# Performance work log

Hardware: AMD Instinct MI355X
Metric: run time of the kernel (lower is better)

## Reference

```python
import jax, jax.numpy as jnp
import numpy as np

B, NA, NE = 1024, 15, 16
N_AGENTS = NA + 1
BN = B * N_AGENTS
D_OWN = D_ALL = D_EN = 32
H, NH, NMOVE, RD = 256, 4, 6, 8
HD = H // NH
GATE = 1.0
NEG = -1e9  # stand-in for -inf (safe under autodiff)


def _gelu(x):
    return jax.nn.gelu(x, approximate=False)  # torch nn.GELU default is exact


def _ln(x, g, b, eps=1e-5):
    m = x.mean(-1, keepdims=True)
    v = ((x - m) ** 2).mean(-1, keepdims=True)
    return (x - m) * jax.lax.rsqrt(v + eps) * g + b


def _masked_mean(x, mask, axis):
    w = mask[..., None].astype(x.dtype)
    return (x * w).sum(axis) / jnp.clip(w.sum(axis), 1e-8)


def _mha(q, kv, mask, Wq, Wk, Wv, Wo):
    # q: [BN,H], kv: [BN,M,H], mask: [BN,M] bool
    bn = q.shape[0]
    qh = (q @ Wq.T).reshape(bn, NH, HD)
    kh = (kv @ Wk.T).reshape(bn, -1, NH, HD)
    vh = (kv @ Wv.T).reshape(bn, -1, NH, HD)
    scores = jnp.einsum('bhd,bmhd->bhm', qh, kh) / np.sqrt(HD)
    scores = jnp.where(mask[:, None, :], scores, NEG)
    attn = jax.nn.softmax(scores, axis=-1)
    ctx = jnp.einsum('bhm,bmhd->bhd', attn, vh).reshape(bn, H)
    return ctx @ Wo.T


def setup_inputs() -> dict:
    key = jax.random.key(0)
    ks = iter(jax.random.split(key, 64))
    nrm = lambda *s: jax.random.normal(next(ks), s, dtype=jnp.float32)
    w = lambda o, i: nrm(o, i) * 0.02
    inp = dict(
        bs=B,
        own_feats=nrm(BN, 1, D_OWN),
        ally_feats=nrm(BN, NA, D_ALL),
        enemy_feats=nrm(BN, NE, D_EN),
        hidden_state=nrm(B, N_AGENTS, H),
        own_W=w(H, D_OWN), own_b=jnp.zeros(H),
        ally_W=w(H, D_ALL), ally_b=jnp.zeros(H),
        en_W=w(H, D_EN), en_b=jnp.zeros(H),
        aA_Wq=w(H, H), aA_Wk=w(H, H), aA_Wv=w(H, H), aA_Wo=w(H, H),
        aE_Wq=w(H, H), aE_Wk=w(H, H), aE_Wv=w(H, H), aE_Wo=w(H, H),
        fuse_W1=w(H, 3 * H), fuse_b1=jnp.zeros(H), fuse_g1=jnp.ones(H), fuse_be1=jnp.zeros(H),
        fuse_W2=w(H, H), fuse_b2=jnp.zeros(H),
        pool_W1=w(128, 3 * H), pool_b1=jnp.zeros(128), pool_g1=jnp.ones(128), pool_be1=jnp.zeros(128),
        pool_W2=w(128, 128), pool_b2=jnp.zeros(128),
        role_W1=w(128, 128), role_b1=jnp.zeros(128), role_g1=jnp.ones(128), role_be1=jnp.zeros(128),
        role_W2=w(RD, 128), role_b2=jnp.zeros(RD),
        rln_g=jnp.ones(RD), rln_b=jnp.zeros(RD),
        gru_Wih=w(3 * H, H + RD), gru_Whh=w(3 * H, H),
        gru_bih=jnp.zeros(3 * H), gru_bhh=jnp.zeros(3 * H),
        qn_W=w(NMOVE, H), qn_b=jnp.zeros(NMOVE),
        qp_W=w(H, H + RD), kp_W=w(H, H),
    )
    return inp


def reference(bs, own_feats, ally_feats, enemy_feats, hidden_state,
              own_W, own_b, ally_W, ally_b, en_W, en_b,
              aA_Wq, aA_Wk, aA_Wv, aA_Wo, aE_Wq, aE_Wk, aE_Wv, aE_Wo,
              fuse_W1, fuse_b1, fuse_g1, fuse_be1, fuse_W2, fuse_b2,
              pool_W1, pool_b1, pool_g1, pool_be1, pool_W2, pool_b2,
              role_W1, role_b1, role_g1, role_be1, role_W2, role_b2,
              rln_g, rln_b, gru_Wih, gru_Whh, gru_bih, gru_bhh,
              qn_W, qn_b, qp_W, kp_W):
    ally_mask = ~jnp.all(ally_feats == 0, axis=-1)   # [BN,Na]
    enemy_mask = ~jnp.all(enemy_feats == 0, axis=-1)  # [BN,Ne]

    own_e = own_feats @ own_W.T + own_b        # [BN,1,H]
    ally_e = ally_feats @ ally_W.T + ally_b    # [BN,Na,H]
    enemy_e = enemy_feats @ en_W.T + en_b      # [BN,Ne,H]
    self_emb = own_e[:, 0]                     # [BN,H]

    cA = _mha(self_emb, ally_e, ally_mask, aA_Wq, aA_Wk, aA_Wv, aA_Wo)
    cE = _mha(self_emb, enemy_e, enemy_mask, aE_Wq, aE_Wk, aE_Wv, aE_Wo)

    # fuse MLP: Linear -> GELU -> LN -> Linear
    f_in = jnp.concatenate([self_emb, cA, cE], axis=-1)
    h0 = _ln(_gelu(f_in @ fuse_W1.T + fuse_b1), fuse_g1, fuse_be1) @ fuse_W2.T + fuse_b2

    pA = _masked_mean(ally_e, ally_mask, 1)
    pE = _masked_mean(enemy_e, enemy_mask, 1)
    p_in = jnp.concatenate([self_emb, pA, pE], axis=-1)
    pooled = _ln(_gelu(p_in @ pool_W1.T + pool_b1), pool_g1, pool_be1) @ pool_W2.T + pool_b2
    r = jnp.tanh(_ln(_gelu(pooled @ role_W1.T + role_b1), role_g1, role_be1) @ role_W2.T + role_b2)
    r = _ln(r, rln_g, rln_b)

    # GRUCell (torch convention)
    h_prev = hidden_state.reshape(-1, H)
    x = jnp.concatenate([h0, GATE * r], axis=-1)
    gi = x @ gru_Wih.T + gru_bih
    gh = h_prev @ gru_Whh.T + gru_bhh
    i_r, i_z, i_n = jnp.split(gi, 3, axis=-1)
    h_r, h_z, h_n = jnp.split(gh, 3, axis=-1)
    rg = jax.nn.sigmoid(i_r + h_r)
    zg = jax.nn.sigmoid(i_z + h_z)
    ng = jnp.tanh(i_n + rg * h_n)
    h_cur = (1.0 - zg) * ng + zg * h_prev

    q_normal = h_cur @ qn_W.T + qn_b  # [BN,n_move]

    q_vec = jnp.concatenate([h_cur, GATE * r], axis=-1) @ qp_W.T  # [BN,H]
    k_vec = enemy_e @ kp_W.T                                       # [BN,Ne,H]
    logits = jnp.einsum('bj,bmj->bm', q_vec, k_vec) / np.sqrt(H)
    logits = jnp.where(enemy_mask, logits, NEG)
    denom = jnp.clip(enemy_mask.sum(-1, keepdims=True), 1).astype(logits.dtype)
    mean_valid = jnp.where(enemy_mask, logits, 0.0).sum(-1, keepdims=True) / denom
    q_interact = logits - mean_valid

    Q = jnp.concatenate([q_normal, q_interact], axis=-1)
    h_out = h_cur.reshape(bs, N_AGENTS, H)
    return Q, h_out
```

## Files before the change

kernel.cpp:

```cpp
#include <hip/hip_runtime.h>
#include <hip/hip_bf16.h>


#define MROWS 16384

typedef __attribute__((ext_vector_type(8))) short short8;
typedef __attribute__((ext_vector_type(4))) float float4v;
typedef __attribute__((ext_vector_type(4))) unsigned short ushort4v;
typedef __attribute__((ext_vector_type(2))) unsigned short ushort2v;

__device__ __forceinline__ unsigned short f2b(float f) {
    __hip_bfloat16 h = __float2bfloat16(f);
    return *reinterpret_cast<unsigned short*>(&h);
}
__device__ __forceinline__ float b2f(unsigned short u) {
    __hip_bfloat16 h;
    *reinterpret_cast<unsigned short*>(&h) = u;
    return __bfloat162float(h);
}
__device__ __forceinline__ void gll16(const unsigned short* g, unsigned short* l) {
    __builtin_amdgcn_global_load_lds((const __attribute__((address_space(1))) void*)g,
                                     (__attribute__((address_space(3))) void*)l, 16, 0, 0);
}

__global__ void cvt_misc(const float* __restrict__ hidden, const float* __restrict__ ownf,
                         unsigned short* __restrict__ XG, unsigned short* __restrict__ OWNb,
                         unsigned short* __restrict__ zbuf) {
    int idx = blockIdx.x * 256 + threadIdx.x;
    const int nh = MROWS * 64;
    const int no = MROWS * 8;
    if (idx < nh) {
        int row = idx >> 6, c4 = (idx & 63) * 4;
        float4 v = *(const float4*)(hidden + (size_t)row * 256 + c4);
        ushort4v d = { f2b(v.x), f2b(v.y), f2b(v.z), f2b(v.w) };
        *(ushort4v*)(XG + (size_t)row * 520 + 264 + c4) = d;
    } else if (idx < nh + no) {
        int j = idx - nh;
        int row = j >> 3, c4 = (j & 7) * 4;
        float4 v = *(const float4*)(ownf + (size_t)row * 32 + c4);
        ushort4v d = { f2b(v.x), f2b(v.y), f2b(v.z), f2b(v.w) };
        *(ushort4v*)(OWNb + (size_t)row * 32 + c4) = d;
    } else if (idx < nh + no + 16) {
        int j = idx - nh - no;
        ((uint4*)zbuf)[j] = make_uint4(0u, 0u, 0u, 0u);
    }
}

struct TOp {
    int type;
    const float* A; int sAi, sAk;
    const float* B; int sBj, sBk;
    void* O; int sOi;
    int I, J, K;
    int nb; int aB, bB, oB;
};
struct TOpSet { int n; int tiles[26]; TOp ops[26]; };

__global__ __launch_bounds__(256)
void compose_tiled(TOpSet S) {
    int t = blockIdx.x;
    int op = 0;
    while (op < S.n && t >= S.tiles[op]) { t -= S.tiles[op]; op++; }
    if (op >= S.n) return;
    TOp o = S.ops[op];
    int ti = (o.I + 31) >> 5, tj = (o.J + 31) >> 5;
    int per = ti * tj;
    int b = t / per;
    int rem = t - b * per;
    int i0 = (rem / tj) * 32, j0 = (rem % tj) * 32;
    int tid = threadIdx.x;
    if (o.type >= 2) {
        for (int e = tid; e < 1024; e += 256) {
            int r = e >> 5, c = e & 31;
            int i = i0 + r, j = j0 + c;
            if (i < o.I && j < o.J) {
                unsigned short v = 0;
                if (o.type == 2) v = f2b(o.A[(long)b * o.aB + (long)i * o.sAi + (long)j * o.sAk]);
                ((unsigned short*)o.O)[(long)b * o.oB + (long)i * o.sOi + j] = v;
            }
        }
        return;
    }
    __shared__ float As[32][33];
    __shared__ float Bs[32][33];
    int tx = tid & 15, ty = tid >> 4;
    float a00 = 0.f, a01 = 0.f, a10 = 0.f, a11 = 0.f;
    const float* Ab = o.A + (long)b * o.aB;
    const float* Bb = o.B + (long)b * o.bB;
    for (int k0 = 0; k0 < o.K; k0 += 32) {
        for (int e = tid; e < 1024; e += 256) {
            int r = e >> 5, c = e & 31;
            As[r][c] = (i0 + r < o.I && k0 + c < o.K)
                       ? Ab[(long)(i0 + r) * o.sAi + (long)(k0 + c) * o.sAk] : 0.f;
            Bs[r][c] = (k0 + r < o.K && j0 + c < o.J)
                       ? Bb[(long)(j0 + c) * o.sBj + (long)(k0 + r) * o.sBk] : 0.f;
        }
        __syncthreads();
#pragma unroll
        for (int k = 0; k < 32; k++) {
            float x0 = As[ty * 2][k], x1 = As[ty * 2 + 1][k];
            float y0 = Bs[k][tx * 2], y1 = Bs[k][tx * 2 + 1];
            a00 += x0 * y0; a01 += x0 * y1; a10 += x1 * y0; a11 += x1 * y1;
        }
        __syncthreads();
    }
    int i = i0 + ty * 2, j = j0 + tx * 2;
    float vals[2][2] = {{a00, a01}, {a10, a11}};
#pragma unroll
    for (int di = 0; di < 2; di++)
#pragma unroll
        for (int dj = 0; dj < 2; dj++) {
            int ii = i + di, jj = j + dj;
            if (ii < o.I && jj < o.J) {
                long oidx = (long)b * o.oB + (long)ii * o.sOi + jj;
                if (o.type == 0) ((unsigned short*)o.O)[oidx] = f2b(vals[di][dj]);
                else ((float*)o.O)[oidx] = vals[di][dj];
            }
        }
}

struct MOp { const float* A; int sAi; const float* x; const float* b1; const float* b2; float* out; int I, K; };
struct MOpSet { int n; int waves[10]; MOp ops[10]; };

__global__ void mv_ops(MOpSet S) {
    int wid = blockIdx.x * 4 + (threadIdx.x >> 6);
    int lane = threadIdx.x & 63;
    int op = 0;
    while (op < S.n && wid >= S.waves[op]) { wid -= S.waves[op]; op++; }
    if (op >= S.n) return;
    MOp o = S.ops[op];
    float s = 0.f;
    for (int k = lane; k < o.K; k += 64) s += o.A[(long)wid * o.sAi + k] * o.x[k];
    for (int off = 32; off; off >>= 1) s += __shfl_xor(s, off, 64);
    if (lane == 0) {
        if (o.b1) s += o.b1[wid];
        if (o.b2) s += o.b2[wid];
        o.out[wid] = s;
    }
}

__global__ __launch_bounds__(256, 4)
void gemm_bf16(const unsigned short* __restrict__ A, int lda,
               const unsigned short* __restrict__ W,
               const float* __restrict__ bias,
               unsigned short* __restrict__ C, int ldc,
               int N, int K, int act,
               const unsigned short* __restrict__ zbuf) {
    __shared__ __align__(16) unsigned short As[128 * 64];
    __shared__ __align__(16) unsigned short Bs[128 * 64];
    int tid = threadIdx.x;
    int m0 = blockIdx.x * 128, n0 = blockIdx.y * 128;
    int wave = tid >> 6, lane = tid & 63;
    int wm = (wave & 1) * 64, wn = (wave >> 1) * 64;
    int l16 = lane & 15, quad = lane >> 4;

    float4v acc[4][4];
#pragma unroll
    for (int i = 0; i < 4; i++)
#pragma unroll
        for (int j = 0; j < 4; j++) acc[i][j] = (float4v){0.f, 0.f, 0.f, 0.f};

    const unsigned short* Aptr[4];
    const unsigned short* Wptr[4];
    int cOff[4];
    unsigned short* ldsA[4];
    unsigned short* ldsB[4];
#pragma unroll
    for (int j = 0; j < 4; j++) {
        int row = wave * 8 + j * 32 + (lane >> 3);
        int cg = (lane & 7) ^ (row & 7);
        cOff[j] = cg * 8;
        Aptr[j] = A + (size_t)(m0 + row) * lda + cg * 8;
        Wptr[j] = (n0 + row < N) ? W + (size_t)(n0 + row) * K + cg * 8 : nullptr;
        ldsA[j] = As + (size_t)(wave * 64 + j * 256) * 8;
        ldsB[j] = Bs + (size_t)(wave * 64 + j * 256) * 8;
    }
    int swz = (l16 & 7) * 8;

    for (int k0 = 0; k0 < K; k0 += 64) {
#pragma unroll
        for (int j = 0; j < 4; j++) {
            int ka = k0 + cOff[j];
            gll16((ka < K) ? Aptr[j] + k0 : zbuf, ldsA[j]);
            gll16((ka < K && Wptr[j]) ? Wptr[j] + k0 : zbuf, ldsB[j]);
        }
        __syncthreads();
#pragma unroll
        for (int kk = 0; kk < 2; kk++) {
            short8 a[4], b[4];
#pragma unroll
            for (int i = 0; i < 4; i++) {
                int ra = wm + i * 16 + l16;
                int rb = wn + i * 16 + l16;
                int co = (kk * 4 + quad) * 8;
                a[i] = *(const short8*)(&As[ra * 64 + (co ^ swz)]);
                b[i] = *(const short8*)(&Bs[rb * 64 + (co ^ swz)]);
            }
#pragma unroll
            for (int i = 0; i < 4; i++)
#pragma unroll
                for (int j2 = 0; j2 < 4; j2++)
                    acc[i][j2] = __builtin_amdgcn_mfma_f32_16x16x32_bf16(a[i], b[j2], acc[i][j2], 0, 0, 0);
        }
        __syncthreads();
    }
#pragma unroll
    for (int i = 0; i < 4; i++) {
#pragma unroll
        for (int j = 0; j < 4; j++) {
#pragma unroll
            for (int rr = 0; rr < 4; rr++) {
                int rowm = m0 + wm + i * 16 + quad * 4 + rr;
                int coln = wn + j * 16 + l16;
                if (n0 + coln >= N) continue;
                float v = acc[i][j][rr];
                if (bias) v += bias[n0 + coln];
                if (act == 1) v = 0.5f * v * (1.f + erff(v * 0.70710678f));
                C[(size_t)rowm * ldc + n0 + coln] = f2b(v);
            }
        }
    }
}

__global__ __launch_bounds__(256)
void ln_fp(const unsigned short* __restrict__ FPC,
           const float* __restrict__ g1, const float* __restrict__ be1,
           const float* __restrict__ g2, const float* __restrict__ be2,
           unsigned short* __restrict__ XG, unsigned short* __restrict__ T2) {
    int tid = threadIdx.x;
    size_t row = (size_t)blockIdx.x * 4 + (tid >> 6);
    int l = tid & 63;
    const unsigned short* src = FPC + row * 384;
    ushort4v vf = *(const ushort4v*)(src + l * 4);
    ushort2v vp = *(const ushort2v*)(src + 256 + l * 2);
    float f0 = b2f(vf[0]), f1 = b2f(vf[1]), f2v = b2f(vf[2]), f3 = b2f(vf[3]);
    float p0 = b2f(vp[0]), p1 = b2f(vp[1]);
    float s = f0 + f1 + f2v + f3;
    float q = f0 * f0 + f1 * f1 + f2v * f2v + f3 * f3;
    float s2 = p0 + p1, q2 = p0 * p0 + p1 * p1;
    for (int o = 32; o; o >>= 1) {
        s += __shfl_xor(s, o, 64); q += __shfl_xor(q, o, 64);
        s2 += __shfl_xor(s2, o, 64); q2 += __shfl_xor(q2, o, 64);
    }
    float mean = s * (1.f / 256.f);
    float rstd = rsqrtf(q * (1.f / 256.f) - mean * mean + 1e-5f);
    float4 g = *(const float4*)(g1 + l * 4);
    float4 be = *(const float4*)(be1 + l * 4);
    ushort4v o4;
    o4[0] = f2b((f0 - mean) * rstd * g.x + be.x);
    o4[1] = f2b((f1 - mean) * rstd * g.y + be.y);
    o4[2] = f2b((f2v - mean) * rstd * g.z + be.z);
    o4[3] = f2b((f3 - mean) * rstd * g.w + be.w);
    *(ushort4v*)(XG + row * 520 + l * 4) = o4;
    float mean2 = s2 * (1.f / 128.f);
    float rstd2 = rsqrtf(q2 * (1.f / 128.f) - mean2 * mean2 + 1e-5f);
    float2 gg = *(const float2*)(g2 + l * 2);
    float2 bb = *(const float2*)(be2 + l * 2);
    ushort2v o2;
    o2[0] = f2b((p0 - mean2) * rstd2 * gg.x + bb.x);
    o2[1] = f2b((p1 - mean2) * rstd2 * gg.y + bb.y);
    *(ushort2v*)(T2 + row * 128 + l * 2) = o2;
}

__global__ __launch_bounds__(256)
void glue_attn(const float* __restrict__ allyf, const float* __restrict__ enemyf,
               const float* __restrict__ ownf, const unsigned short* __restrict__ QKS,
               unsigned short* __restrict__ X) {
    __shared__ __align__(16) float af[4][540];
    __shared__ __align__(16) float ef[4][576];
    __shared__ __align__(16) float qk[4][288];
    __shared__ float attnA[4][64];
    __shared__ float attnE[4][64];
    __shared__ float mskA[4][16];
    __shared__ float mskE[4][16];
    int tid = threadIdx.x;
    size_t rb = (size_t)blockIdx.x * 4;

    for (int idx = tid; idx < 480; idx += 256) {
        int r = idx / 120, ch = idx - r * 120;
        float4 v = *(const float4*)(allyf + ((rb + r) * 480 + ch * 4));
        *(float4*)&af[r][(ch >> 3) * 36 + (ch & 7) * 4] = v;
    }
    for (int idx = tid; idx < 512; idx += 256) {
        int r = idx >> 7, ch = idx & 127;
        float4 v = *(const float4*)(enemyf + ((rb + r) * 512 + ch * 4));
        *(float4*)&ef[r][(ch >> 3) * 36 + (ch & 7) * 4] = v;
    }
    if (tid < 128) {
        int r = tid >> 5, ch = tid & 31;
        short8 v = *(const short8*)(QKS + (rb + r) * 256 + ch * 8);
#pragma unroll
        for (int j = 0; j < 8; j++)
            qk[r][(ch >> 2) * 36 + (ch & 3) * 8 + j] = b2f((unsigned short)v[j]);
    } else {
        int r = (tid - 128) >> 5, c = (tid - 128) & 31;
        X[(rb + r) * 360 + c] = f2b(ownf[(rb + r) * 32 + c]);
    }
    if (tid < 24) {
        int r = tid / 6, c = 98 + tid % 6;
        X[(rb + r) * 360 + c] = 0;
    }
    __syncthreads();

    if (tid < 248) {
        int pair = tid >> 1, half = tid & 1;
        int r = pair / 31, e = pair - r * 31;
        const float* base = (e < 15) ? &af[r][e * 36] : &ef[r][(e - 15) * 36];
        const float4* b4 = (const float4*)base + half * 4;
        bool nz = false;
#pragma unroll
        for (int k = 0; k < 4; k++) {
            float4 v = b4[k];
            nz |= (v.x != 0.f) || (v.y != 0.f) || (v.z != 0.f) || (v.w != 0.f);
        }
        int other = __shfl_xor((int)nz, 1, 64);
        float mv = (nz || other != 0) ? 1.f : 0.f;
        if (half == 0) {
            if (e < 15) mskA[r][e] = mv; else mskE[r][e - 15] = mv;
        }
    } else if (tid < 252) {
        mskA[tid - 248][15] = 0.f;
    }
    __syncthreads();

    int r = tid >> 6, lane = tid & 63;
    int h = lane >> 4, m = lane & 15;
    {
        float sc = -3.0e38f;
        if (m < 15) {
            const float4* qa = (const float4*)&qk[r][h * 36];
            const float4* aa = (const float4*)&af[r][m * 36];
            float s = 0.f;
#pragma unroll
            for (int k = 0; k < 8; k++) {
                float4 q = qa[k], a = aa[k];
                s += q.x * a.x + q.y * a.y + q.z * a.z + q.w * a.w;
            }
            sc = (mskA[r][m] > 0.f) ? s * 0.125f : -1e9f;
        }
        float mx = sc;
        for (int o = 8; o; o >>= 1) mx = fmaxf(mx, __shfl_xor(mx, o, 64));
        float e = (m < 15) ? __expf(sc - mx) : 0.f;
        float sm = e;
        for (int o = 8; o; o >>= 1) sm += __shfl_xor(sm, o, 64);
        attnA[r][h * 16 + m] = e / sm;
    }
    {
        const float4* qa = (const float4*)&qk[r][(4 + h) * 36];
        const float4* aa = (const float4*)&ef[r][m * 36];
        float s = 0.f;
#pragma unroll
        for (int k = 0; k < 8; k++) {
            float4 q = qa[k], a = aa[k];
            s += q.x * a.x + q.y * a.y + q.z * a.z + q.w * a.w;
        }
        float sc = (mskE[r][m] > 0.f) ? s * 0.125f : -1e9f;
        float mx = sc;
        for (int o = 8; o; o >>= 1) mx = fmaxf(mx, __shfl_xor(mx, o, 64));
        float e = __expf(sc - mx);
        float sm = e;
        for (int o = 8; o; o >>= 1) sm += __shfl_xor(sm, o, 64);
        attnE[r][h * 16 + m] = e / sm;
    }
    __syncthreads();
    size_t row = rb + r;
#pragma unroll
    for (int it = 0; it < 2; it++) {
        int idx = lane + it * 64;
        int hh = idx >> 5, c = idx & 31;
        float sA = 0.f;
        for (int mm = 0; mm < 15; mm++) sA += attnA[r][hh * 16 + mm] * af[r][mm * 36 + c];
        X[row * 360 + 104 + idx] = f2b(sA);
        float sE = 0.f;
        for (int mm = 0; mm < 16; mm++) sE += attnE[r][hh * 16 + mm] * ef[r][mm * 36 + c];
        X[row * 360 + 232 + idx] = f2b(sE);
    }
    if (lane < 32) {
        float cnt = 0.f;
        for (int mm = 0; mm < 15; mm++) cnt += mskA[r][mm];
        float s = 0.f;
        for (int mm = 0; mm < 15; mm++) s += af[r][mm * 36 + lane];
        X[row * 360 + 32 + lane] = f2b(s / fmaxf(cnt, 1e-8f));
        if (lane == 0) X[row * 360 + 96] = f2b(cnt > 0.f ? 1.f : 0.f);
    } else {
        int c = lane - 32;
        float cnt = 0.f;
        for (int mm = 0; mm < 16; mm++) cnt += mskE[r][mm];
        float s = 0.f;
        for (int mm = 0; mm < 16; mm++) s += ef[r][mm * 36 + c];
        X[row * 360 + 64 + c] = f2b(s / fmaxf(cnt, 1e-8f));
        if (c == 0) X[row * 360 + 97] = f2b(cnt > 0.f ? 1.f : 0.f);
    }
}

__global__ __launch_bounds__(256)
void ln_role(const unsigned short* __restrict__ T3, const float* __restrict__ g1,
             const float* __restrict__ be1, const float* __restrict__ W2,
             const float* __restrict__ b2, const float* __restrict__ rg,
             const float* __restrict__ rb, unsigned short* __restrict__ XG) {
    __shared__ float t3[32][132];
    __shared__ float gl[128], bl[128];
    int tid = threadIdx.x;
    size_t base = (size_t)blockIdx.x * 4096;
    for (int idx = tid; idx < 4096; idx += 256)
        t3[idx >> 7][idx & 127] = b2f(T3[base + idx]);
    if (tid < 128) { gl[tid] = g1[tid]; bl[tid] = be1[tid]; }
    __syncthreads();
    int r = tid >> 3, t = tid & 7;
    float s = 0.f, q = 0.f;
    for (int c = 0; c < 16; c++) { float v = t3[r][t * 16 + c]; s += v; q += v * v; }
    for (int o = 4; o; o >>= 1) { s += __shfl_xor(s, o, 8); q += __shfl_xor(q, o, 8); }
    float mean = s * (1.f / 128.f);
    float var = q * (1.f / 128.f) - mean * mean;
    float rstd = rsqrtf(var + 1e-5f);
    float acc = b2[t];
    const float* w = W2 + t * 128;
    for (int d = 0; d < 128; d++)
        acc += w[d] * ((t3[r][d] - mean) * rstd * gl[d] + bl[d]);
    float v = tanhf(acc);
    float mn = v;
    for (int o = 4; o; o >>= 1) mn += __shfl_xor(mn, o, 8);
    mn *= 0.125f;
    float dv = v - mn, qq = dv * dv;
    for (int o = 4; o; o >>= 1) qq += __shfl_xor(qq, o, 8);
    qq *= 0.125f;
    size_t row = (size_t)blockIdx.x * 32 + r;
    XG[row * 520 + 256 + t] = f2b(dv * rsqrtf(qq + 1e-5f) * rg[t] + rb[t]);
}

__global__ __launch_bounds__(256)
void glue_gru(const unsigned short* __restrict__ G, const float* __restrict__ hp,
              float* __restrict__ hout, unsigned short* __restrict__ XQ,
              const unsigned short* __restrict__ XG) {
    int tid = threadIdx.x;
    size_t row = (size_t)blockIdx.x * 4 + (tid >> 6);
    int l = tid & 63;
    size_t b = row * 1024;
    ushort4v vr = *(const ushort4v*)(G + b + l * 4);
    ushort4v vz = *(const ushort4v*)(G + b + 256 + l * 4);
    ushort4v vi = *(const ushort4v*)(G + b + 512 + l * 4);
    ushort4v vh = *(const ushort4v*)(G + b + 768 + l * 4);
    float4 hv = *(const float4*)(hp + row * 256 + l * 4);
    float hpv[4] = {hv.x, hv.y, hv.z, hv.w};
    float hov[4];
    ushort4v xq;
#pragma unroll
    for (int j = 0; j < 4; j++) {
        float rg = 1.f / (1.f + __expf(-b2f(vr[j])));
        float zg = 1.f / (1.f + __expf(-b2f(vz[j])));
        float ng = tanhf(b2f(vi[j]) + rg * b2f(vh[j]));
        float h = (1.f - zg) * ng + zg * hpv[j];
        hov[j] = h;
        xq[j] = f2b(h);
    }
    *(float4*)(hout + row * 256 + l * 4) = make_float4(hov[0], hov[1], hov[2], hov[3]);
    *(ushort4v*)(XQ + row * 264 + l * 4) = xq;
    if (l < 2)
        ((ushort4v*)(XQ + row * 264 + 256))[l] = ((const ushort4v*)(XG + row * 520 + 256))[l];
}

__global__ __launch_bounds__(256)
void glue_final(const unsigned short* __restrict__ QWS, const float* __restrict__ efeats,
                const float* __restrict__ qnb, float* __restrict__ Q) {
    __shared__ __align__(16) float ef[8][576];
    __shared__ __align__(16) float qw[8][40];
    int tid = threadIdx.x;
    size_t rb = (size_t)blockIdx.x * 8;
    for (int idx = tid; idx < 1024; idx += 256) {
        int r = idx >> 7, ch = idx & 127;
        float4 v = *(const float4*)(efeats + (rb + r) * 512 + ch * 4);
        *(float4*)&ef[r][(ch >> 3) * 36 + (ch & 7) * 4] = v;
    }
    for (int idx = tid; idx < 320; idx += 256) {
        int r = idx / 40, c = idx % 40;
        qw[r][c] = b2f(QWS[(rb + r) * 40 + c]);
    }
    __syncthreads();
    int r = tid >> 5, t = tid & 31;
    size_t row = rb + r;
    float lg = 0.f, mk = 0.f;
    if (t < 16) {
        const float4* fr = (const float4*)&ef[r][t * 36];
        const float4* qv = (const float4*)&qw[r][0];
        bool nz = false;
        float s = 0.f;
#pragma unroll
        for (int k = 0; k < 8; k++) {
            float4 a = fr[k], b = qv[k];
            nz |= (a.x != 0.f) || (a.y != 0.f) || (a.z != 0.f) || (a.w != 0.f);
            s += a.x * b.x + a.y * b.y + a.z * b.z + a.w * b.w;
        }
        mk = nz ? 1.f : 0.f;
        lg = (s + qw[r][32]) * 0.0625f;
    }
    float sv = mk * lg, cv = mk;
    for (int o = 8; o; o >>= 1) { sv += __shfl_xor(sv, o, 64); cv += __shfl_xor(cv, o, 64); }
    float mean = sv / fmaxf(cv, 1.f);
    if (t < 16) Q[row * 22 + 6 + t] = (mk > 0.f ? lg : -1e9f) - mean;
    if (t < 6) Q[row * 22 + t] = qw[r][33 + t] + qnb[t];
}

extern "C" void kernel_launch(void* const* d_in, const int* in_sizes, int n_in,
                              void* d_out, int out_size, void* d_ws, size_t ws_size,
                              hipStream_t stream) {
    const float* own_feats = (const float*)d_in[1];
    const float* ally_feats = (const float*)d_in[2];
    const float* enemy_feats = (const float*)d_in[3];
    const float* hidden = (const float*)d_in[4];
    const float* own_W = (const float*)d_in[5];   const float* own_b = (const float*)d_in[6];
    const float* ally_W = (const float*)d_in[7];  const float* ally_b = (const float*)d_in[8];
    const float* en_W = (const float*)d_in[9];    const float* en_b = (const float*)d_in[10];
    const float* aA_Wq = (const float*)d_in[11];  const float* aA_Wk = (const float*)d_in[12];
    const float* aA_Wv = (const float*)d_in[13];  const float* aA_Wo = (const float*)d_in[14];
    const float* aE_Wq = (const float*)d_in[15];  const float* aE_Wk = (const float*)d_in[16];
    const float* aE_Wv = (const float*)d_in[17];  const float* aE_Wo = (const float*)d_in[18];
    const float* fuse_W1 = (const float*)d_in[19]; const float* fuse_b1 = (const float*)d_in[20];
    const float* fuse_g1 = (const float*)d_in[21]; const float* fuse_be1 = (const float*)d_in[22];
    const float* fuse_W2 = (const float*)d_in[23]; const float* fuse_b2 = (const float*)d_in[24];
    const float* pool_W1 = (const float*)d_in[25]; const float* pool_b1 = (const float*)d_in[26];
    const float* pool_g1 = (const float*)d_in[27]; const float* pool_be1 = (const float*)d_in[28];
    const float* pool_W2 = (const float*)d_in[29]; const float* pool_b2 = (const float*)d_in[30];
    const float* role_W1 = (const float*)d_in[31]; const float* role_b1 = (const float*)d_in[32];
    const float* role_g1 = (const float*)d_in[33]; const float* role_be1 = (const float*)d_in[34];
    const float* role_W2 = (const float*)d_in[35]; const float* role_b2 = (const float*)d_in[36];
    const float* rln_g = (const float*)d_in[37];   const float* rln_b = (const float*)d_in[38];
    const float* gru_Wih = (const float*)d_in[39]; const float* gru_Whh = (const float*)d_in[40];
    const float* gru_bih = (const float*)d_in[41]; const float* gru_bhh = (const float*)d_in[42];
    const float* qn_W = (const float*)d_in[43];    const float* qn_b = (const float*)d_in[44];
    const float* qp_W = (const float*)d_in[45];    const float* kp_W = (const float*)d_in[46];

    char* wsp = (char*)d_ws;
    size_t off = 0;
    auto alloc = [&](size_t bytes) { void* p = wsp + off; off = (off + bytes + 255) & ~(size_t)255; return p; };

    unsigned short* X    = (unsigned short*)alloc((size_t)MROWS * 360 * 2);
    unsigned short* XG   = (unsigned short*)alloc((size_t)MROWS * 520 * 2);
    unsigned short* FPC  = (unsigned short*)alloc((size_t)MROWS * 384 * 2);
    unsigned short* GIb  = (unsigned short*)alloc((size_t)MROWS * 1024 * 2);
    unsigned short* XQ   = (unsigned short*)alloc((size_t)MROWS * 264 * 2);
    unsigned short* T2b  = (unsigned short*)alloc((size_t)MROWS * 128 * 2);
    unsigned short* T3b  = (unsigned short*)alloc((size_t)MROWS * 128 * 2);
    unsigned short* QKSb = (unsigned short*)alloc((size_t)MROWS * 256 * 2);
    unsigned short* QWSb = (unsigned short*)alloc((size_t)MROWS * 40 * 2);
    unsigned short* OWNb = (unsigned short*)alloc((size_t)MROWS * 32 * 2);
    unsigned short* FPW  = (unsigned short*)alloc(384 * 360 * 2);
    unsigned short* WGRU = (unsigned short*)alloc(1024 * 520 * 2);
    unsigned short* QWSW = (unsigned short*)alloc(40 * 264 * 2);
    unsigned short* WQKSO= (unsigned short*)alloc(256 * 32 * 2);
    unsigned short* rpW  = (unsigned short*)alloc(128 * 128 * 2);
    unsigned short* zbuf = (unsigned short*)alloc(256);
    float* WkAp = (float*)alloc(256 * 32 * 4);
    float* WvAp = (float*)alloc(256 * 32 * 4);
    float* WkEp = (float*)alloc(256 * 32 * 4);
    float* WvEp = (float*)alloc(256 * 32 * 4);
    float* Wkpp = (float*)alloc(256 * 32 * 4);
    float* WQKS_AE = (float*)alloc(256 * 256 * 4);
    float* WoVA = (float*)alloc(256 * 128 * 4);
    float* WoVE = (float*)alloc(256 * 128 * 4);
    float* bvAp = (float*)alloc(256 * 4);
    float* bvEp = (float*)alloc(256 * 4);
    float* bkpp = (float*)alloc(256 * 4);
    float* vall = (float*)alloc(768 * 4);
    float* qksb = (float*)alloc(256 * 4);
    float* fpb  = (float*)alloc(384 * 4);
    float* gbias= (float*)alloc(1024 * 4);
    float* rpb  = (float*)alloc(128 * 4);

    float* Qout = (float*)d_out;
    float* Hout = Qout + (size_t)MROWS * 22;

    auto tilesOf = [](const TOp& o) {
        return o.nb * (((o.I + 31) / 32) * ((o.J + 31) / 32));
    };

    cvt_misc<<<(MROWS * 64 + MROWS * 8 + 16 + 255) / 256, 256, 0, stream>>>(hidden, own_feats, XG, OWNb, zbuf);

    {
        MOpSet S; S.n = 5; int waves = 0;
        S.ops[0] = {aA_Wv, 256, ally_b, nullptr, nullptr, bvAp, 256, 256};
        S.ops[1] = {aE_Wv, 256, en_b, nullptr, nullptr, bvEp, 256, 256};
        S.ops[2] = {kp_W, 256, en_b, nullptr, nullptr, bkpp, 256, 256};
        S.ops[3] = {nullptr, 0, nullptr, own_b, nullptr, vall, 256, 0};
        S.ops[4] = {role_W1, 128, pool_b2, role_b1, nullptr, rpb, 128, 128};
        for (int i = 0; i < S.n; i++) { S.waves[i] = S.ops[i].I; waves += S.ops[i].I; }
        mv_ops<<<(waves + 3) / 4, 256, 0, stream>>>(S);
    }
    {
        TOpSet S; S.n = 0; int grid = 0;
        auto add = [&](TOp o) { S.tiles[S.n] = tilesOf(o); grid += S.tiles[S.n]; S.ops[S.n++] = o; };
        add({1, aA_Wk, 256, 1, ally_W, 1, 32, WkAp, 32, 256, 32, 256, 1, 0, 0, 0});
        add({1, aA_Wv, 256, 1, ally_W, 1, 32, WvAp, 32, 256, 32, 256, 1, 0, 0, 0});
        add({1, aE_Wk, 256, 1, en_W, 1, 32, WkEp, 32, 256, 32, 256, 1, 0, 0, 0});
        add({1, aE_Wv, 256, 1, en_W, 1, 32, WvEp, 32, 256, 32, 256, 1, 0, 0, 0});
        add({1, kp_W, 256, 1, en_W, 1, 32, Wkpp, 32, 256, 32, 256, 1, 0, 0, 0});
        compose_tiled<<<grid, 256, 0, stream>>>(S);
    }
    {
        TOpSet S; S.n = 0; int grid = 0;
        auto add = [&](TOp o) { S.tiles[S.n] = tilesOf(o); grid += S.tiles[S.n]; S.ops[S.n++] = o; };
        add({1, WkAp, 1, 32, aA_Wq, 1, 256, WQKS_AE, 256, 32, 256, 64, 4, 2048, 16384, 8192});
        add({1, WkEp, 1, 32, aE_Wq, 1, 256, WQKS_AE + 128 * 256, 256, 32, 256, 64, 4, 2048, 16384, 8192});
        add({1, aA_Wo, 256, 1, WvAp, 1, 32, WoVA, 128, 256, 32, 64, 4, 64, 2048, 32});
        add({1, aE_Wo, 256, 1, WvEp, 1, 32, WoVE, 128, 256, 32, 64, 4, 64, 2048, 32});
        compose_tiled<<<grid, 256, 0, stream>>>(S);
    }
    {
        MOpSet S; S.n = 3; int waves = 0;
        S.ops[0] = {aA_Wo, 256, bvAp, nullptr, nullptr, vall + 256, 256, 256};
        S.ops[1] = {aE_Wo, 256, bvEp, nullptr, nullptr, vall + 512, 256, 256};
        S.ops[2] = {WQKS_AE, 256, own_b, nullptr, nullptr, qksb, 256, 256};
        for (int i = 0; i < S.n; i++) { S.waves[i] = S.ops[i].I; waves += S.ops[i].I; }
        mv_ops<<<(waves + 3) / 4, 256, 0, stream>>>(S);
    }
    {
        MOpSet S; S.n = 5; int waves = 0;
        S.ops[0] = {fuse_W1, 768, vall, fuse_b1, nullptr, fpb, 256, 768};
        S.ops[1] = {pool_W1, 768, vall, pool_b1, nullptr, fpb + 256, 128, 256};
        S.ops[2] = {gru_Wih, 264, fuse_b2, gru_bih, gru_bhh, gbias, 512, 256};
        S.ops[3] = {gru_Wih + 512 * 264, 264, fuse_b2, gru_bih + 512, nullptr, gbias + 512, 256, 256};
        S.ops[4] = {nullptr, 0, nullptr, gru_bhh + 512, nullptr, gbias + 768, 256, 0};
        for (int i = 0; i < S.n; i++) { S.waves[i] = S.ops[i].I; waves += S.ops[i].I; }
        mv_ops<<<(waves + 3) / 4, 256, 0, stream>>>(S);
    }
    {
        TOpSet S; S.n = 0; int grid = 0;
        auto add = [&](TOp o) { S.tiles[S.n] = tilesOf(o); grid += S.tiles[S.n]; S.ops[S.n++] = o; };
        add({0, fuse_W1, 768, 1, own_W, 1, 32, FPW, 360, 256, 32, 256, 1, 0, 0, 0});
        add({3, nullptr, 0, 0, nullptr, 0, 0, FPW + 32, 360, 256, 72, 0, 1, 0, 0, 0});
        add({0, fuse_W1 + 256, 768, 1, WoVA, 1, 128, FPW + 104, 360, 256, 128, 256, 1, 0, 0, 0});
        add({0, fuse_W1 + 512, 768, 1, WoVE, 1, 128, FPW + 232, 360, 256, 128, 256, 1, 0, 0, 0});
        add({0, pool_W1, 768, 1, own_W, 1, 32, FPW + 256 * 360, 360, 128, 32, 256, 1, 0, 0, 0});
        add({0, pool_W1 + 256, 768, 1, ally_W, 1, 32, FPW + 256 * 360 + 32, 360, 128, 32, 256, 1, 0, 0, 0});
        add({0, pool_W1 + 512, 768, 1, en_W, 1, 32, FPW + 256 * 360 + 64, 360, 128, 32, 256, 1, 0, 0, 0});
        add({0, pool_W1 + 256, 768, 1, ally_b, 0, 1, FPW + 256 * 360 + 96, 360, 128, 1, 256, 1, 0, 0, 0});
        add({0, pool_W1 + 512, 768, 1, en_b, 0, 1, FPW + 256 * 360 + 97, 360, 128, 1, 256, 1, 0, 0, 0});
        add({3, nullptr, 0, 0, nullptr, 0, 0, FPW + 256 * 360 + 98, 360, 128, 262, 0, 1, 0, 0, 0});
        add({0, gru_Wih, 264, 1, fuse_W2, 1, 256, WGRU, 520, 512, 256, 256, 1, 0, 0, 0});
        add({2, gru_Wih + 256, 264, 1, nullptr, 0, 0, WGRU + 256, 520, 512, 8, 0, 1, 0, 0, 0});
        add({2, gru_Whh, 256, 1, nullptr, 0, 0, WGRU + 264, 520, 512, 256, 0, 1, 0, 0, 0});
        add({0, gru_Wih + 512 * 264, 264, 1, fuse_W2, 1, 256, WGRU + 512 * 520, 520, 256, 256, 256, 1, 0, 0, 0});
        add({2, gru_Wih + 512 * 264 + 256, 264, 1, nullptr, 0, 0, WGRU + 512 * 520 + 256, 520, 256, 8, 0, 1, 0, 0, 0});
        add({3, nullptr, 0, 0, nullptr, 0, 0, WGRU + 512 * 520 + 264, 520, 256, 256, 0, 1, 0, 0, 0});
        add({3, nullptr, 0, 0, nullptr, 0, 0, WGRU + 768 * 520, 520, 256, 264, 0, 1, 0, 0, 0});
        add({2, gru_Whh + 512 * 256, 256, 1, nullptr, 0, 0, WGRU + 768 * 520 + 264, 520, 256, 256, 0, 1, 0, 0, 0});
        add({0, Wkpp, 1, 32, qp_W, 1, 264, QWSW, 264, 32, 264, 256, 1, 0, 0, 0});
        add({0, bkpp, 0, 1, qp_W, 1, 264, QWSW + 32 * 264, 264, 1, 264, 256, 1, 0, 0, 0});
        add({2, qn_W, 256, 1, nullptr, 0, 0, QWSW + 33 * 264, 264, 6, 256, 0, 1, 0, 0, 0});
        add({3, nullptr, 0, 0, nullptr, 0, 0, QWSW + 33 * 264 + 256, 264, 6, 8, 0, 1, 0, 0, 0});
        add({3, nullptr, 0, 0, nullptr, 0, 0, QWSW + 39 * 264, 264, 1, 264, 0, 1, 0, 0, 0});
        add({0, WQKS_AE, 256, 1, own_W, 1, 32, WQKSO, 32, 256, 32, 256, 1, 0, 0, 0});
        add({0, role_W1, 128, 1, pool_W2, 1, 128, rpW, 128, 128, 128, 128, 1, 0, 0, 0});
        compose_tiled<<<grid, 256, 0, stream>>>(S);
    }

    auto gemm = [&](const unsigned short* A, int lda, const unsigned short* Wm, const float* bias,
                    unsigned short* C, int ldc, int N, int K, int act) {
        gemm_bf16<<<dim3(MROWS / 128, (N + 127) / 128), 256, 0, stream>>>(A, lda, Wm, bias, C, ldc, N, K, act, zbuf);
    };

    gemm(OWNb, 32, WQKSO, qksb, QKSb, 256, 256, 32, 0);
    glue_attn<<<MROWS / 4, 256, 0, stream>>>(ally_feats, enemy_feats, own_feats, QKSb, X);
    gemm(X, 360, FPW, fpb, FPC, 384, 384, 360, 1);
    ln_fp<<<MROWS / 4, 256, 0, stream>>>(FPC, fuse_g1, fuse_be1, pool_g1, pool_be1, XG, T2b);
    gemm(T2b, 128, rpW, rpb, T3b, 128, 128, 128, 1);
    ln_role<<<MROWS / 32, 256, 0, stream>>>(T3b, role_g1, role_be1, role_W2, role_b2, rln_g, rln_b, XG);
    gemm(XG, 520, WGRU, gbias, GIb, 1024, 1024, 520, 0);
    glue_gru<<<MROWS / 4, 256, 0, stream>>>(GIb, hidden, Hout, XQ, XG);
    gemm(XQ, 264, QWSW, nullptr, QWSb, 40, 40, 264, 0);
    glue_final<<<MROWS / 8, 256, 0, stream>>>(QWSb, enemy_feats, qn_b, Qout);
}
```

Before: 448.0 us.

## Double-buffer GEMM LDS tiles with BK=32 to overlap loads and MFMA

Restructures the bf16 GEMM main loop to use two 128x32 LDS buffers per operand and issue the next tile's global-to-LDS loads before computing the current tile. This halves the K-step and replaces the two syncthreads per step with one waitcnt plus barrier, so memory latency can be hidden behind MFMA work. The swizzle pattern changes to match the 32-wide rows. It risks more barriers per unit of K and a single-barrier scheme that only holds if the reads from one buffer finish before it is overwritten.

Result: no change. 453.6 us (+1.2%).

```diff
diff --git a/kernel.cpp b/kernel.cpp
--- a/kernel.cpp
+++ b/kernel.cpp
@@ -146,8 +146,8 @@
                unsigned short* __restrict__ C, int ldc,
                int N, int K, int act,
                const unsigned short* __restrict__ zbuf) {
-    __shared__ __align__(16) unsigned short As[128 * 64];
-    __shared__ __align__(16) unsigned short Bs[128 * 64];
+    __shared__ __align__(16) unsigned short As[2][128 * 32];
+    __shared__ __align__(16) unsigned short Bs[2][128 * 32];
     int tid = threadIdx.x;
     int m0 = blockIdx.x * 128, n0 = blockIdx.y * 128;
     int wave = tid >> 6, lane = tid & 63;
@@ -160,50 +160,58 @@
 #pragma unroll
         for (int j = 0; j < 4; j++) acc[i][j] = (float4v){0.f, 0.f, 0.f, 0.f};
 
-    const unsigned short* Aptr[4];
-    const unsigned short* Wptr[4];
-    int cOff[4];
-    unsigned short* ldsA[4];
-    unsigned short* ldsB[4];
-#pragma unroll
-    for (int j = 0; j < 4; j++) {
-        int row = wave * 8 + j * 32 + (lane >> 3);
-        int cg = (lane & 7) ^ (row & 7);
+    const unsigned short* Aptr[2];
+    const unsigned short* Wptr[2];
+    int cOff[2];
+    int ldsOff[2];
+#pragma unroll
+    for (int j = 0; j < 2; j++) {
+        int row = wave * 16 + j * 64 + (lane >> 2);
+        int cg = (lane & 3) ^ ((row >> 1) & 3);
         cOff[j] = cg * 8;
         Aptr[j] = A + (size_t)(m0 + row) * lda + cg * 8;
         Wptr[j] = (n0 + row < N) ? W + (size_t)(n0 + row) * K + cg * 8 : nullptr;
-        ldsA[j] = As + (size_t)(wave * 64 + j * 256) * 8;
-        ldsB[j] = Bs + (size_t)(wave * 64 + j * 256) * 8;
-    }
-    int swz = (l16 & 7) * 8;
-
-    for (int k0 = 0; k0 < K; k0 += 64) {
-#pragma unroll
-        for (int j = 0; j < 4; j++) {
+        ldsOff[j] = (wave * 64 + j * 256) * 8;
+    }
+    int swz = ((l16 >> 1) & 3) * 8;
+    int nt = (K + 31) >> 5;
+
+    auto stage = [&](int buf, int k0) {
+#pragma unroll
+        for (int j = 0; j < 2; j++) {
             int ka = k0 + cOff[j];
-            gll16((ka < K) ? Aptr[j] + k0 : zbuf, ldsA[j]);
-            gll16((ka < K && Wptr[j]) ? Wptr[j] + k0 : zbuf, ldsB[j]);
-        }
-        __syncthreads();
-#pragma unroll
-        for (int kk = 0; kk < 2; kk++) {
-            short8 a[4], b[4];
-#pragma unroll
-            for (int i = 0; i < 4; i++) {
-                int ra = wm + i * 16 + l16;
-                int rb = wn + i * 16 + l16;
-                int co = (kk * 4 + quad) * 8;
-                a[i] = *(const short8*)(&As[ra * 64 + (co ^ swz)]);
-                b[i] = *(const short8*)(&Bs[rb * 64 + (co ^ swz)]);
-            }
-#pragma unroll
-            for (int i = 0; i < 4; i++)
-#pragma unroll
-                for (int j2 = 0; j2 < 4; j2++)
-                    acc[i][j2] = __builtin_amdgcn_mfma_f32_16x16x32_bf16(a[i], b[j2], acc[i][j2], 0, 0, 0);
-        }
-        __syncthreads();
-    }
+            gll16((ka < K) ? Aptr[j] + k0 : zbuf, &As[buf][ldsOff[j]]);
+            gll16((ka < K && Wptr[j]) ? Wptr[j] + k0 : zbuf, &Bs[buf][ldsOff[j]]);
+        }
+    };
+    auto compute = [&](int buf) {
+        short8 a[4], b[4];
+#pragma unroll
+        for (int i = 0; i < 4; i++) {
+            int ra = (wm + i * 16 + l16) * 32;
+            int rb = (wn + i * 16 + l16) * 32;
+            int co = quad * 8;
+            a[i] = *(const short8*)(&As[buf][ra + (co ^ swz)]);
+            b[i] = *(const short8*)(&Bs[buf][rb + (co ^ swz)]);
+        }
+#pragma unroll
+        for (int i = 0; i < 4; i++)
+#pragma unroll
+            for (int j2 = 0; j2 < 4; j2++)
+                acc[i][j2] = __builtin_amdgcn_mfma_f32_16x16x32_bf16(a[i], b[j2], acc[i][j2], 0, 0, 0);
+    };
+
+    stage(0, 0);
+    asm volatile("s_waitcnt vmcnt(0)" ::: "memory");
+    __builtin_amdgcn_s_barrier();
+    for (int t = 0; t < nt - 1; t++) {
+        stage((t + 1) & 1, (t + 1) << 5);
+        compute(t & 1);
+        asm volatile("s_waitcnt vmcnt(0)" ::: "memory");
+        __builtin_amdgcn_s_barrier();
+    }
+    compute((nt - 1) & 1);
+
 #pragma unroll
     for (int i = 0; i < 4; i++) {
 #pragma unroll
```
